# Optimization experiments

Measured on AMD Instinct MI355X. Metric: run time of the kernel, lower is better.

## Reference

```python
import jax, jax.numpy as jnp
import numpy as np

H = 8        # num_heads
DK = 128     # head_k_dim
DV = 128     # head_v_dim
HID = 1024   # hidden_size
CHUNK = 64   # chunk size for chunked linear attention
EPS = 1e-5


def setup_inputs() -> dict:
    key = jax.random.key(0)
    ks = jax.random.split(key, 16)
    s = 0.02
    inp = {
        "hidden_states": jax.random.normal(ks[0], (2, 8192, HID), dtype=jnp.float32),
        "Wq": jax.random.normal(ks[1], (HID, HID), dtype=jnp.float32) * s,
        "Wk": jax.random.normal(ks[2], (HID, HID), dtype=jnp.float32) * s,
        "Wv": jax.random.normal(ks[3], (HID, HID), dtype=jnp.float32) * s,
        "fmq_w1": jax.random.normal(ks[4], (DK, DK), dtype=jnp.float32) * s,
        "fmq_b1": jnp.zeros((DK,), dtype=jnp.float32),
        "fmq_w2": jax.random.normal(ks[5], (DK, DK), dtype=jnp.float32) * s,
        "fmq_b2": jnp.zeros((DK,), dtype=jnp.float32),
        "fmk_w1": jax.random.normal(ks[6], (DK, DK), dtype=jnp.float32) * s,
        "fmk_b1": jnp.zeros((DK,), dtype=jnp.float32),
        "fmk_w2": jax.random.normal(ks[7], (DK, DK), dtype=jnp.float32) * s,
        "fmk_b2": jnp.zeros((DK,), dtype=jnp.float32),
        "rms_w": jnp.ones((DV,), dtype=jnp.float32),
        "Wo": jax.random.normal(ks[8], (HID, HID), dtype=jnp.float32) * s,
    }
    return inp


def reference(hidden_states, Wq, Wk, Wv, fmq_w1, fmq_b1, fmq_w2, fmq_b2,
              fmk_w1, fmk_b1, fmk_w2, fmk_b2, rms_w, Wo):
    B, T, _ = hidden_states.shape
    scale = DK ** -0.5

    # projections (torch Linear: x @ W.T), split heads -> [B,T,H,D]
    q = (hidden_states @ Wq.T).reshape(B, T, H, DK)
    k = (hidden_states @ Wk.T).reshape(B, T, H, DK)
    v = (hidden_states @ Wv.T).reshape(B, T, H, DV)

    # Hadamard feature maps: l1(x) * l2(x)
    q = (q @ fmq_w1.T + fmq_b1) * (q @ fmq_w2.T + fmq_b2)
    k = (k @ fmk_w1.T + fmk_b1) * (k @ fmk_w2.T + fmk_b2)

    q = q * scale

    # chunked causal linear attention: o_t = q_t @ sum_{s<=t} k_s v_s^T
    N = T // CHUNK
    qc = q.reshape(B, N, CHUNK, H, DK)
    kc = k.reshape(B, N, CHUNK, H, DK)
    vc = v.reshape(B, N, CHUNK, H, DV)

    # per-chunk KV outer-product sums, exclusive prefix over chunks
    kv = jnp.einsum('bnchk,bnchv->bnhkv', kc, vc)
    S = jnp.cumsum(kv, axis=1) - kv  # state entering each chunk

    o_inter = jnp.einsum('bnchk,bnhkv->bnchv', qc, S)

    # intra-chunk causal part
    A = jnp.einsum('bnihk,bnjhk->bnhij', qc, kc)
    causal = jnp.tril(jnp.ones((CHUNK, CHUNK), dtype=bool))
    A = jnp.where(causal, A, 0.0)
    o_intra = jnp.einsum('bnhij,bnjhv->bnihv', A, vc)

    o = (o_inter + o_intra).reshape(B, T, H, DV)

    # RMSNorm over head_v_dim with affine weight
    o = o * jax.lax.rsqrt(jnp.mean(o * o, axis=-1, keepdims=True) + EPS) * rms_w

    o = o.reshape(B, T, H * DV) @ Wo.T
    return o
```

## Files before the change

kernel.cpp:

```cpp
#include <hip/hip_runtime.h>


typedef __bf16 bf16x8 __attribute__((ext_vector_type(8)));
typedef float  f32x4  __attribute__((ext_vector_type(4)));

__device__ __forceinline__ float bf2f(unsigned short u) {
  union { unsigned int i; float f; } v; v.i = ((unsigned int)u) << 16; return v.f;
}
__device__ __forceinline__ unsigned short f2bf(float f) {
  union { float f; unsigned int i; } v; v.f = f;
  return (unsigned short)((v.i + 0x8000u) >> 16);
}
__device__ __forceinline__ unsigned int pk2(float a, float b) {
  union { float f; unsigned int i; } x, y; x.f = a; y.f = b;
  return ((x.i + 0x8000u) >> 16) | ((y.i + 0x8000u) & 0xFFFF0000u);
}
__device__ __forceinline__ f32x4 mfma16(bf16x8 a, bf16x8 b, f32x4 c) {
  return __builtin_amdgcn_mfma_f32_16x16x32_bf16(a, b, c, 0, 0, 0);
}
__device__ __forceinline__ void gl_lds16(const unsigned short* g, unsigned short* l) {
  __builtin_amdgcn_global_load_lds((const __attribute__((address_space(1))) void*)g,
                                   (__attribute__((address_space(3))) void*)l, 16, 0, 0);
}

__global__ void __launch_bounds__(256)
cvt_kernel(const float* __restrict__ s, unsigned short* __restrict__ d, int n4) {
  const int i = blockIdx.x * 256 + threadIdx.x;
  if (i >= n4) return;
  const float4 f = ((const float4*)s)[i];
  uint2 o; o.x = pk2(f.x, f.y); o.y = pk2(f.z, f.w);
  ((uint2*)d)[i] = o;
}
__global__ void __launch_bounds__(256)
cvt4_kernel(const float* __restrict__ s0, const float* __restrict__ s1,
            const float* __restrict__ s2, const float* __restrict__ s3,
            unsigned short* __restrict__ d0, unsigned short* __restrict__ d1,
            unsigned short* __restrict__ d2, unsigned short* __restrict__ d3,
            int n4) {
  const int w = blockIdx.y;
  const float* s = (w == 0) ? s0 : (w == 1) ? s1 : (w == 2) ? s2 : s3;
  unsigned short* d = (w == 0) ? d0 : (w == 1) ? d1 : (w == 2) ? d2 : d3;
  const int i = blockIdx.x * 256 + threadIdx.x;
  if (i >= n4) return;
  const float4 f = ((const float4*)s)[i];
  uint2 o; o.x = pk2(f.x, f.y); o.y = pk2(f.z, f.w);
  ((uint2*)d)[i] = o;
}

__global__ void __launch_bounds__(256)
qkv_gemm(const unsigned short* __restrict__ Xb,
         const unsigned short* __restrict__ Wqb, const unsigned short* __restrict__ Wkb,
         const unsigned short* __restrict__ Wvb,
         unsigned short* __restrict__ Q, unsigned short* __restrict__ Kf,
         unsigned short* __restrict__ VT) {
  constexpr int K = 1024;
  __shared__ unsigned short As[128 * 32];
  __shared__ unsigned short Bs[128 * 32];
  const int tid = threadIdx.x;
  const int bx = blockIdx.x;
  const int rowBase = blockIdx.y * 128;
  const int sel = bx >> 3;
  const int colBase = (bx & 7) * 128;
  const unsigned short* Bw = (sel == 0) ? Wqb : ((sel == 1) ? Wkb : Wvb);

  const int lane = tid & 63, wid = tid >> 6;
  const int lq = lane & 15, quad = lane >> 4;
  const int wm = (wid >> 1) * 64, wn = (wid & 1) * 64;

  const int srow = wid * 32 + (lane >> 2);
  const int scol = (lane & 3) * 8;
  const unsigned short* gA = Xb + (size_t)(rowBase + srow) * K + scol;
  const unsigned short* gB = Bw + (size_t)(colBase + srow) * K + scol;
  unsigned short* lA0 = As + wid * 1024;
  unsigned short* lA1 = As + wid * 1024 + 512;
  unsigned short* lB0 = Bs + wid * 1024;
  unsigned short* lB1 = Bs + wid * 1024 + 512;

  f32x4 acc[4][4] = {};
  for (int kt = 0; kt < K / 32; ++kt) {
    __syncthreads();
    gl_lds16(gA + kt * 32, lA0);
    gl_lds16(gA + kt * 32 + 16 * K, lA1);
    gl_lds16(gB + kt * 32, lB0);
    gl_lds16(gB + kt * 32 + 16 * K, lB1);
    __syncthreads();
    bf16x8 af[4], bfr[4];
#pragma unroll
    for (int i = 0; i < 4; ++i)
      af[i] = *(const bf16x8*)(As + (wm + i * 16 + lq) * 32 + quad * 8);
#pragma unroll
    for (int j = 0; j < 4; ++j)
      bfr[j] = *(const bf16x8*)(Bs + (wn + j * 16 + lq) * 32 + quad * 8);
#pragma unroll
    for (int i = 0; i < 4; ++i)
#pragma unroll
      for (int j = 0; j < 4; ++j) acc[i][j] = mfma16(af[i], bfr[j], acc[i][j]);
  }
  if (sel < 2) {
    unsigned short* C = (sel == 0) ? Q : Kf;
#pragma unroll
    for (int i = 0; i < 4; ++i)
#pragma unroll
      for (int j = 0; j < 4; ++j) {
        const int col = colBase + wn + j * 16 + lq;
#pragma unroll
        for (int r = 0; r < 4; ++r) {
          const int row = rowBase + wm + i * 16 + quad * 4 + r;
          C[(size_t)row * 1024 + col] = f2bf(acc[i][j][r]);
        }
      }
  } else {
#pragma unroll
    for (int i = 0; i < 4; ++i)
#pragma unroll
      for (int j = 0; j < 4; ++j) {
        const int col = colBase + wn + j * 16 + lq;
        const int h = col >> 7, dv = col & 127;
        const int row0 = rowBase + wm + i * 16 + quad * 4;
        const int b = row0 >> 13, tl = row0 & 8191;
        ushort4 t4;
        t4.x = f2bf(acc[i][j][0]); t4.y = f2bf(acc[i][j][1]);
        t4.z = f2bf(acc[i][j][2]); t4.w = f2bf(acc[i][j][3]);
        *(ushort4*)(VT + (((size_t)(b * 8 + h) * 128 + dv) << 13) + tl) = t4;
      }
  }
}

__global__ void __launch_bounds__(256)
out_gemm(const unsigned short* __restrict__ A, const unsigned short* __restrict__ Bw,
         float* __restrict__ C) {
  constexpr int K = 1024;
  __shared__ unsigned short As[128 * 32];
  __shared__ unsigned short Bs[128 * 32];
  const int tid = threadIdx.x;
  const int rowBase = blockIdx.y * 128;
  const int colBase = blockIdx.x * 128;
  const int lane = tid & 63, wid = tid >> 6;
  const int lq = lane & 15, quad = lane >> 4;
  const int wm = (wid >> 1) * 64, wn = (wid & 1) * 64;

  const int srow = wid * 32 + (lane >> 2);
  const int scol = (lane & 3) * 8;
  const unsigned short* gA = A + (size_t)(rowBase + srow) * K + scol;
  const unsigned short* gB = Bw + (size_t)(colBase + srow) * K + scol;
  unsigned short* lA0 = As + wid * 1024;
  unsigned short* lA1 = As + wid * 1024 + 512;
  unsigned short* lB0 = Bs + wid * 1024;
  unsigned short* lB1 = Bs + wid * 1024 + 512;

  f32x4 acc[4][4] = {};
  for (int kt = 0; kt < K / 32; ++kt) {
    __syncthreads();
    gl_lds16(gA + kt * 32, lA0);
    gl_lds16(gA + kt * 32 + 16 * K, lA1);
    gl_lds16(gB + kt * 32, lB0);
    gl_lds16(gB + kt * 32 + 16 * K, lB1);
    __syncthreads();
    bf16x8 af[4], bfr[4];
#pragma unroll
    for (int i = 0; i < 4; ++i)
      af[i] = *(const bf16x8*)(As + (wm + i * 16 + lq) * 32 + quad * 8);
#pragma unroll
    for (int j = 0; j < 4; ++j)
      bfr[j] = *(const bf16x8*)(Bs + (wn + j * 16 + lq) * 32 + quad * 8);
#pragma unroll
    for (int i = 0; i < 4; ++i)
#pragma unroll
      for (int j = 0; j < 4; ++j) acc[i][j] = mfma16(af[i], bfr[j], acc[i][j]);
  }
#pragma unroll
  for (int i = 0; i < 4; ++i)
#pragma unroll
    for (int j = 0; j < 4; ++j) {
      const int col = colBase + wn + j * 16 + lq;
#pragma unroll
      for (int r = 0; r < 4; ++r) {
        const int row = rowBase + wm + i * 16 + quad * 4 + r;
        C[(size_t)row * 1024 + col] = acc[i][j][r];
      }
    }
}

__global__ void __launch_bounds__(256)
fm_kernel(unsigned short* __restrict__ Qb, unsigned short* __restrict__ Kb,
          const unsigned short* __restrict__ fq1b, const unsigned short* __restrict__ fq2b,
          const unsigned short* __restrict__ fk1b, const unsigned short* __restrict__ fk2b,
          const float* __restrict__ fqb1, const float* __restrict__ fqb2,
          const float* __restrict__ fkb1, const float* __restrict__ fkb2) {
  __shared__ unsigned short Aq[64 * 136];
  const int z = blockIdx.z;
  unsigned short* buf = z ? Kb : Qb;
  const unsigned short* w1b = z ? fk1b : fq1b;
  const unsigned short* w2b = z ? fk2b : fq2b;
  const float* b1 = z ? fkb1 : fqb1;
  const float* b2 = z ? fkb2 : fqb2;
  const float scale = z ? 1.0f : 0.08838834764831843f;

  const int tid = threadIdx.x;
  const int t0 = blockIdx.x * 256;
  const int h = blockIdx.y, hc = h * 128;
  const int lane = tid & 63, wid = tid >> 6, lq = lane & 15, quad = lane >> 4;
  const int wn = wid * 32;

  bf16x8 w1f[4][2], w2f[4][2];
#pragma unroll
  for (int ks = 0; ks < 4; ++ks)
#pragma unroll
    for (int j = 0; j < 2; ++j) {
      const int nr = wn + j * 16 + lq;
      w1f[ks][j] = *(const bf16x8*)(w1b + nr * 128 + ks * 32 + quad * 8);
      w2f[ks][j] = *(const bf16x8*)(w2b + nr * 128 + ks * 32 + quad * 8);
    }

  const float bb1[2] = { b1[wn + lq], b1[wn + 16 + lq] };
  const float bb2[2] = { b2[wn + lq], b2[wn + 16 + lq] };

  for (int tt = 0; tt < 4; ++tt) {
    const int tb = t0 + tt * 64;
#pragma unroll
    for (int it = 0; it < 4; ++it) {
      const int p = tid + it * 256;
      const int row = p >> 4, c8 = (p & 15) * 8;
      *(uint4*)(Aq + row * 136 + c8) =
          *(const uint4*)(buf + (size_t)(tb + row) * 1024 + hc + c8);
    }
    __syncthreads();
    f32x4 a1[4][2] = {}, a2[4][2] = {};
#pragma unroll
    for (int ks = 0; ks < 4; ++ks) {
      bf16x8 af[4];
#pragma unroll
      for (int i = 0; i < 4; ++i)
        af[i] = *(const bf16x8*)(Aq + (i * 16 + lq) * 136 + ks * 32 + quad * 8);
#pragma unroll
      for (int j = 0; j < 2; ++j)
#pragma unroll
        for (int i = 0; i < 4; ++i) {
          a1[i][j] = mfma16(af[i], w1f[ks][j], a1[i][j]);
          a2[i][j] = mfma16(af[i], w2f[ks][j], a2[i][j]);
        }
    }
    __syncthreads();
#pragma unroll
    for (int j = 0; j < 2; ++j) {
      const int col = wn + j * 16 + lq;
#pragma unroll
      for (int i = 0; i < 4; ++i)
#pragma unroll
        for (int r = 0; r < 4; ++r) {
          const float v = (a1[i][j][r] + bb1[j]) * (a2[i][j][r] + bb2[j]) * scale;
          buf[(size_t)(tb + i * 16 + quad * 4 + r) * 1024 + hc + col] = f2bf(v);
        }
    }
  }
}

__global__ void __launch_bounds__(256)
kv_kernel(const unsigned short* __restrict__ Kf, const unsigned short* __restrict__ VT,
          unsigned short* __restrict__ KV) {
  __shared__ unsigned short Kt[128 * 72];
  __shared__ unsigned short Vt[128 * 72];
  const int tid = threadIdx.x;
  const int n = blockIdx.x, bh = blockIdx.y;
  const int b = bh >> 3, h = bh & 7;
  const int t0g = b * 8192 + n * 64;
  const int tl0 = n * 64;
#pragma unroll
  for (int it = 0; it < 4; ++it) {
    const int p = tid + it * 256;
    const int d = p >> 3, c8 = (p & 7) * 8;
    *(uint4*)(Vt + d * 72 + c8) =
        *(const uint4*)(VT + (((size_t)bh * 128 + d) << 13) + tl0 + c8);
    const int tok = p >> 4, c8k = (p & 15) * 8;
    const unsigned short* src = Kf + (size_t)(t0g + tok) * 1024 + h * 128 + c8k;
    ushort4 k0 = *(const ushort4*)(src);
    ushort4 k1 = *(const ushort4*)(src + 4);
    Kt[(c8k + 0) * 72 + tok] = k0.x; Kt[(c8k + 1) * 72 + tok] = k0.y;
    Kt[(c8k + 2) * 72 + tok] = k0.z; Kt[(c8k + 3) * 72 + tok] = k0.w;
    Kt[(c8k + 4) * 72 + tok] = k1.x; Kt[(c8k + 5) * 72 + tok] = k1.y;
    Kt[(c8k + 6) * 72 + tok] = k1.z; Kt[(c8k + 7) * 72 + tok] = k1.w;
  }
  __syncthreads();
  const int lane = tid & 63, wid = tid >> 6, lq = lane & 15, quad = lane >> 4;
  const int wm = (wid >> 1) * 64, wn = (wid & 1) * 64;
  f32x4 acc[4][4] = {};
#pragma unroll
  for (int ks = 0; ks < 2; ++ks) {
    bf16x8 af[4], bfr[4];
#pragma unroll
    for (int i = 0; i < 4; ++i)
      af[i] = *(const bf16x8*)(Vt + (wm + i * 16 + lq) * 72 + ks * 32 + quad * 8);
#pragma unroll
    for (int j = 0; j < 4; ++j)
      bfr[j] = *(const bf16x8*)(Kt + (wn + j * 16 + lq) * 72 + ks * 32 + quad * 8);
#pragma unroll
    for (int i = 0; i < 4; ++i)
#pragma unroll
      for (int j = 0; j < 4; ++j) acc[i][j] = mfma16(af[i], bfr[j], acc[i][j]);
  }
  const size_t base = ((size_t)bh * 128 + n) * 16384;
#pragma unroll
  for (int i = 0; i < 4; ++i)
#pragma unroll
    for (int j = 0; j < 4; ++j)
#pragma unroll
      for (int r = 0; r < 4; ++r)
        KV[base + (size_t)(wm + i * 16 + quad * 4 + r) * 128 + wn + j * 16 + lq] =
            f2bf(acc[i][j][r]);
}

__global__ void __launch_bounds__(256)
cumsum_kernel(unsigned short* __restrict__ KV) {
  const int idx = blockIdx.x * 256 + threadIdx.x;
  const int bh = idx >> 14, e = idx & 16383;
  unsigned short* p = KV + (size_t)bh * (128 * 16384) + e;
  float run = 0.f;
  for (int n = 0; n < 128; ++n) {
    const float x = bf2f(*p);
    *p = f2bf(run);
    run += x;
    p += 16384;
  }
}

__global__ void __launch_bounds__(256)
attn_kernel(const unsigned short* __restrict__ Q, const unsigned short* __restrict__ Kf,
            const unsigned short* __restrict__ VT, const unsigned short* __restrict__ S,
            const float* __restrict__ rmsw, unsigned short* __restrict__ O) {
  __shared__ uint4 smem4[3968];
  unsigned short* sm = (unsigned short*)smem4;
  unsigned short* SQ = sm;
  unsigned short* KS = sm + 8704;
  unsigned short* VTl = sm + 17920;
  unsigned short* AL = sm + 27136;
  float* OL = (float*)sm;
  float* RED = (float*)AL;
  float* SCL = RED + 256;

  const int tid = threadIdx.x;
  const int n = blockIdx.x, bh = blockIdx.y;
  const int b = bh >> 3, h = bh & 7;
  const int t0g = b * 8192 + n * 64;
  const int tl0 = n * 64;
  const int lane = tid & 63, wid = tid >> 6, lq = lane & 15, quad = lane >> 4;

#pragma unroll
  for (int it = 0; it < 4; ++it) {
    const int p = tid + it * 256;
    const int row = p >> 4, c8 = (p & 15) * 8;
    *(uint4*)(SQ + row * 136 + c8) =
        *(const uint4*)(Q + (size_t)(t0g + row) * 1024 + h * 128 + c8);
    *(uint4*)(KS + row * 136 + c8) =
        *(const uint4*)(Kf + (size_t)(t0g + row) * 1024 + h * 128 + c8);
    const int d = p >> 3, c8b = (p & 7) * 8;
    *(uint4*)(VTl + d * 72 + c8b) =
        *(const uint4*)(VT + (((size_t)bh * 128 + d) << 13) + tl0 + c8b);
  }
  __syncthreads();

  {
    f32x4 aa[4] = {};
#pragma unroll
    for (int ks = 0; ks < 4; ++ks) {
      bf16x8 kf = *(const bf16x8*)(KS + (wid * 16 + lq) * 136 + ks * 32 + quad * 8);
#pragma unroll
      for (int i = 0; i < 4; ++i) {
        bf16x8 qf = *(const bf16x8*)(SQ + (i * 16 + lq) * 136 + ks * 32 + quad * 8);
        aa[i] = mfma16(qf, kf, aa[i]);
      }
    }
#pragma unroll
    for (int i = 0; i < 4; ++i)
#pragma unroll
      for (int r = 0; r < 4; ++r) {
        const int qp = i * 16 + quad * 4 + r, kp = wid * 16 + lq;
        AL[qp * 72 + kp] = f2bf(kp <= qp ? aa[i][r] : 0.f);
      }
  }
  __syncthreads();

  const size_t sbase = ((size_t)bh * 128 + n) * 16384;
#pragma unroll
  for (int it = 0; it < 4; ++it) {
    const int p = tid + it * 256;
    const int dv = p >> 3, c8 = (p & 7) * 8;
    *(uint4*)(KS + dv * 72 + c8) = *(const uint4*)(S + sbase + (size_t)dv * 128 + c8);
  }
  __syncthreads();

  f32x4 oa[4][2] = {};
#pragma unroll
  for (int ks = 0; ks < 2; ++ks) {
    bf16x8 bv[2], sf[2];
#pragma unroll
    for (int j = 0; j < 2; ++j) {
      bv[j] = *(const bf16x8*)(VTl + (wid * 32 + j * 16 + lq) * 72 + ks * 32 + quad * 8);
      sf[j] = *(const bf16x8*)(KS + (wid * 32 + j * 16 + lq) * 72 + ks * 32 + quad * 8);
    }
#pragma unroll
    for (int i = 0; i < 4; ++i) {
      bf16x8 af = *(const bf16x8*)(AL + (i * 16 + lq) * 72 + ks * 32 + quad * 8);
      bf16x8 qf = *(const bf16x8*)(SQ + (i * 16 + lq) * 136 + ks * 32 + quad * 8);
#pragma unroll
      for (int j = 0; j < 2; ++j) {
        oa[i][j] = mfma16(af, bv[j], oa[i][j]);
        oa[i][j] = mfma16(qf, sf[j], oa[i][j]);
      }
    }
  }
  __syncthreads();

#pragma unroll
  for (int it = 0; it < 4; ++it) {
    const int p = tid + it * 256;
    const int dv = p >> 3, c8 = (p & 7) * 8;
    *(uint4*)(KS + dv * 72 + c8) =
        *(const uint4*)(S + sbase + (size_t)dv * 128 + 64 + c8);
  }
  __syncthreads();

#pragma unroll
  for (int ks = 0; ks < 2; ++ks) {
    bf16x8 sf[2];
#pragma unroll
    for (int j = 0; j < 2; ++j)
      sf[j] = *(const bf16x8*)(KS + (wid * 32 + j * 16 + lq) * 72 + ks * 32 + quad * 8);
#pragma unroll
    for (int i = 0; i < 4; ++i) {
      bf16x8 qf = *(const bf16x8*)(SQ + (i * 16 + lq) * 136 + (ks + 2) * 32 + quad * 8);
#pragma unroll
      for (int j = 0; j < 2; ++j) oa[i][j] = mfma16(qf, sf[j], oa[i][j]);
    }
  }
  __syncthreads();

#pragma unroll
  for (int i = 0; i < 4; ++i)
#pragma unroll
    for (int j = 0; j < 2; ++j)
#pragma unroll
      for (int r = 0; r < 4; ++r)
        OL[(i * 16 + quad * 4 + r) * 132 + wid * 32 + j * 16 + lq] = oa[i][j][r];
  __syncthreads();

  {
    const int r = tid >> 2, part = tid & 3;
    const float* pr = OL + r * 132 + part * 32;
    float s = 0.f;
#pragma unroll
    for (int c = 0; c < 32; ++c) { const float v = pr[c]; s += v * v; }
    RED[r * 4 + part] = s;
  }
  __syncthreads();
  if (tid < 64) {
    const float ms = (RED[tid * 4] + RED[tid * 4 + 1] + RED[tid * 4 + 2] + RED[tid * 4 + 3]) *
                     (1.f / 128.f);
    SCL[tid] = rsqrtf(ms + 1e-5f);
  }
  __syncthreads();

#pragma unroll
  for (int it = 0; it < 4; ++it) {
    const int r = (tid >> 4) + it * 16;
    const int c8 = (tid & 15) * 8;
    const float sc = SCL[r];
    unsigned short us[8];
#pragma unroll
    for (int e = 0; e < 8; ++e)
      us[e] = f2bf(OL[r * 132 + c8 + e] * sc * rmsw[c8 + e]);
    uint4 pk;
    pk.x = (unsigned int)us[0] | ((unsigned int)us[1] << 16);
    pk.y = (unsigned int)us[2] | ((unsigned int)us[3] << 16);
    pk.z = (unsigned int)us[4] | ((unsigned int)us[5] << 16);
    pk.w = (unsigned int)us[6] | ((unsigned int)us[7] << 16);
    *(uint4*)(O + (size_t)(t0g + r) * 1024 + h * 128 + c8) = pk;
  }
}

extern "C" void kernel_launch(void* const* d_in, const int* in_sizes, int n_in,
                              void* d_out, int out_size, void* d_ws, size_t ws_size,
                              hipStream_t stream) {
  const float* X    = (const float*)d_in[0];
  const float* Wq   = (const float*)d_in[1];
  const float* Wk   = (const float*)d_in[2];
  const float* Wv   = (const float*)d_in[3];
  const float* fq1  = (const float*)d_in[4];
  const float* fqb1 = (const float*)d_in[5];
  const float* fq2  = (const float*)d_in[6];
  const float* fqb2 = (const float*)d_in[7];
  const float* fk1  = (const float*)d_in[8];
  const float* fkb1 = (const float*)d_in[9];
  const float* fk2  = (const float*)d_in[10];
  const float* fkb2 = (const float*)d_in[11];
  const float* rmsw = (const float*)d_in[12];
  const float* Wo   = (const float*)d_in[13];

  const size_t MB = 1u << 20;
  char* ws = (char*)d_ws;
  unsigned short* Q    = (unsigned short*)(ws);
  unsigned short* Kf   = (unsigned short*)(ws + 32 * MB);
  unsigned short* VT   = (unsigned short*)(ws + 64 * MB);
  unsigned short* KV   = (unsigned short*)(ws + 96 * MB);
  unsigned short* Xb   = KV;
  unsigned short* Wqb  = (unsigned short*)(ws + 160 * MB);
  unsigned short* Wkb  = (unsigned short*)(ws + 162 * MB);
  unsigned short* Wvb  = (unsigned short*)(ws + 164 * MB);
  unsigned short* Wob  = (unsigned short*)(ws + 166 * MB);
  unsigned short* fq1b = (unsigned short*)(ws + 168 * MB);
  unsigned short* fq2b = fq1b + 16384;
  unsigned short* fk1b = fq1b + 32768;
  unsigned short* fk2b = fq1b + 49152;
  unsigned short* O    = Q;

  cvt4_kernel<<<dim3(1024, 4), 256, 0, stream>>>(Wq, Wk, Wv, Wo,
                                                 Wqb, Wkb, Wvb, Wob, 262144);
  cvt4_kernel<<<dim3(16, 4), 256, 0, stream>>>(fq1, fq2, fk1, fk2,
                                               fq1b, fq2b, fk1b, fk2b, 4096);
  cvt_kernel<<<16384, 256, 0, stream>>>(X, Xb, 4194304);

  qkv_gemm<<<dim3(24, 128), 256, 0, stream>>>(Xb, Wqb, Wkb, Wvb, Q, Kf, VT);
  fm_kernel<<<dim3(64, 8, 2), 256, 0, stream>>>(Q, Kf, fq1b, fq2b, fk1b, fk2b,
                                                fqb1, fqb2, fkb1, fkb2);
  kv_kernel<<<dim3(128, 16), 256, 0, stream>>>(Kf, VT, KV);
  cumsum_kernel<<<1024, 256, 0, stream>>>(KV);
  attn_kernel<<<dim3(128, 16), 256, 0, stream>>>(Q, Kf, VT, KV, rmsw, O);
  out_gemm<<<dim3(8, 128), 256, 0, stream>>>(O, Wob, (float*)d_out);
}
```

Baseline: 450.6 us.

## Replace QKV and output GEMMs with 256x256 tiles and multi-stage async LDS pipeline

```diff
diff --git a/kernel.cpp b/kernel.cpp
--- a/kernel.cpp
+++ b/kernel.cpp
@@ -1,5 +1,4 @@
 #include <hip/hip_runtime.h>
-
 
 typedef __bf16 bf16x8 __attribute__((ext_vector_type(8)));
 typedef float  f32x4  __attribute__((ext_vector_type(4)));
@@ -47,136 +46,164 @@
   ((uint2*)d)[i] = o;
 }
 
-__global__ void __launch_bounds__(256)
-qkv_gemm(const unsigned short* __restrict__ Xb,
-         const unsigned short* __restrict__ Wqb, const unsigned short* __restrict__ Wkb,
-         const unsigned short* __restrict__ Wvb,
-         unsigned short* __restrict__ Q, unsigned short* __restrict__ Kf,
-         unsigned short* __restrict__ VT) {
-  constexpr int K = 1024;
-  __shared__ unsigned short As[128 * 32];
-  __shared__ unsigned short Bs[128 * 32];
-  const int tid = threadIdx.x;
-  const int bx = blockIdx.x;
-  const int rowBase = blockIdx.y * 128;
-  const int sel = bx >> 3;
-  const int colBase = (bx & 7) * 128;
-  const unsigned short* Bw = (sel == 0) ? Wqb : ((sel == 1) ? Wkb : Wvb);
-
+__device__ __forceinline__ int stage_goff(int s) {
+  const int j = s >> 3, c = (s & 7) ^ (j & 7);
+  return (2 * j + (c >> 2)) * 1024 + (c & 3) * 8;
+}
+
+__device__ __forceinline__ void gemm256_loop(const unsigned short* __restrict__ gA,
+                                             const unsigned short* __restrict__ gB,
+                                             unsigned short* __restrict__ ldsA,
+                                             unsigned short* __restrict__ ldsB,
+                                             int tid, f32x4 (&acc)[8][4]) {
   const int lane = tid & 63, wid = tid >> 6;
   const int lq = lane & 15, quad = lane >> 4;
-  const int wm = (wid >> 1) * 64, wn = (wid & 1) * 64;
-
-  const int srow = wid * 32 + (lane >> 2);
-  const int scol = (lane & 3) * 8;
-  const unsigned short* gA = Xb + (size_t)(rowBase + srow) * K + scol;
-  const unsigned short* gB = Bw + (size_t)(colBase + srow) * K + scol;
-  unsigned short* lA0 = As + wid * 1024;
-  unsigned short* lA1 = As + wid * 1024 + 512;
-  unsigned short* lB0 = Bs + wid * 1024;
-  unsigned short* lB1 = Bs + wid * 1024 + 512;
-
-  f32x4 acc[4][4] = {};
-  for (int kt = 0; kt < K / 32; ++kt) {
-    __syncthreads();
-    gl_lds16(gA + kt * 32, lA0);
-    gl_lds16(gA + kt * 32 + 16 * K, lA1);
-    gl_lds16(gB + kt * 32, lB0);
-    gl_lds16(gB + kt * 32 + 16 * K, lB1);
-    __syncthreads();
+  const int wm = (wid >> 2) * 128, wn = (wid & 3) * 64;
+
+  const unsigned short* gA0 = gA + stage_goff(tid);
+  const unsigned short* gA1 = gA + stage_goff(512 + tid);
+  const unsigned short* gB0 = gB + stage_goff(tid);
+  const unsigned short* gB1 = gB + stage_goff(512 + tid);
+  const int l0 = wid * 512;
+  const int l1 = 4096 + wid * 512;
+  const int soff = (lq >> 1) * 64 + (((((lq & 1) << 2) + quad) ^ ((lq >> 1) & 7))) * 8;
+
+#pragma unroll
+  for (int h = 0; h < 3; ++h) {
+    gl_lds16(gA0 + h * 32, ldsA + h * 8192 + l0);
+    gl_lds16(gA1 + h * 32, ldsA + h * 8192 + l1);
+    gl_lds16(gB0 + h * 32, ldsB + h * 8192 + l0);
+    gl_lds16(gB1 + h * 32, ldsB + h * 8192 + l1);
+  }
+  asm volatile("s_waitcnt vmcnt(8)" ::: "memory");
+  __builtin_amdgcn_s_barrier();
+  __builtin_amdgcn_sched_barrier(0);
+
+#pragma unroll
+  for (int u = 0; u < 32; ++u) {
+    const unsigned short* A8 = ldsA + (u & 3) * 8192;
+    const unsigned short* B8 = ldsB + (u & 3) * 8192;
+    unsigned short* sa = ldsA + ((u + 3) & 3) * 8192;
+    unsigned short* sb = ldsB + ((u + 3) & 3) * 8192;
     bf16x8 af[4], bfr[4];
-#pragma unroll
-    for (int i = 0; i < 4; ++i)
-      af[i] = *(const bf16x8*)(As + (wm + i * 16 + lq) * 32 + quad * 8);
-#pragma unroll
-    for (int j = 0; j < 4; ++j)
-      bfr[j] = *(const bf16x8*)(Bs + (wn + j * 16 + lq) * 32 + quad * 8);
-#pragma unroll
-    for (int i = 0; i < 4; ++i)
-#pragma unroll
-      for (int j = 0; j < 4; ++j) acc[i][j] = mfma16(af[i], bfr[j], acc[i][j]);
-  }
+    if (u < 29) {
+      gl_lds16(gA0 + (u + 3) * 32, sa + l0);
+      gl_lds16(gA1 + (u + 3) * 32, sa + l1);
+    }
+#pragma unroll
+    for (int f = 0; f < 4; ++f)
+      af[f] = *(const bf16x8*)(A8 + (wm + f * 16) * 32 + soff);
+#pragma unroll
+    for (int g = 0; g < 4; ++g)
+      bfr[g] = *(const bf16x8*)(B8 + (wn + g * 16) * 32 + soff);
+    __builtin_amdgcn_s_barrier();
+    __builtin_amdgcn_s_setprio(1);
+#pragma unroll
+    for (int f = 0; f < 4; ++f)
+#pragma unroll
+      for (int g = 0; g < 4; ++g) acc[f][g] = mfma16(af[f], bfr[g], acc[f][g]);
+    __builtin_amdgcn_s_setprio(0);
+    if (u < 29) {
+      gl_lds16(gB0 + (u + 3) * 32, sb + l0);
+      gl_lds16(gB1 + (u + 3) * 32, sb + l1);
+    }
+#pragma unroll
+    for (int f = 0; f < 4; ++f)
+      af[f] = *(const bf16x8*)(A8 + (wm + 64 + f * 16) * 32 + soff);
+    __builtin_amdgcn_s_barrier();
+    __builtin_amdgcn_s_setprio(1);
+#pragma unroll
+    for (int f = 0; f < 4; ++f)
+#pragma unroll
+      for (int g = 0; g < 4; ++g) acc[f + 4][g] = mfma16(af[f], bfr[g], acc[f + 4][g]);
+    __builtin_amdgcn_s_setprio(0);
+    __builtin_amdgcn_sched_barrier(0);
+    if (u < 31) {
+      if (u < 29)       asm volatile("s_waitcnt vmcnt(8)" ::: "memory");
+      else if (u == 29) asm volatile("s_waitcnt vmcnt(4)" ::: "memory");
+      else              asm volatile("s_waitcnt vmcnt(0)" ::: "memory");
+      __builtin_amdgcn_s_barrier();
+      __builtin_amdgcn_sched_barrier(0);
+    }
+  }
+}
+
+__global__ void __launch_bounds__(512, 2)
+qkv_gemm256(const unsigned short* __restrict__ Xb,
+            const unsigned short* __restrict__ Wqb, const unsigned short* __restrict__ Wkb,
+            const unsigned short* __restrict__ Wvb,
+            unsigned short* __restrict__ Q, unsigned short* __restrict__ Kf,
+            unsigned short* __restrict__ VT) {
+  extern __shared__ unsigned short lds[];
+  const int tid = threadIdx.x;
+  const int l = (blockIdx.x & 7) * 96 + (blockIdx.x >> 3);
+  const int tm = l & 63, ct = l >> 6;
+  const int sel = ct >> 2;
+  const int rowBase = tm * 256, colBase = (ct & 3) * 256;
+  const unsigned short* Bw = (sel == 0) ? Wqb : ((sel == 1) ? Wkb : Wvb);
+
+  f32x4 acc[8][4] = {};
+  gemm256_loop(Xb + (size_t)rowBase * 1024, Bw + (size_t)colBase * 1024,
+               lds, lds + 32768, tid, acc);
+
+  const int lane = tid & 63, wid = tid >> 6;
+  const int lq = lane & 15, quad = lane >> 4;
+  const int wm = (wid >> 2) * 128, wn = (wid & 3) * 64;
   if (sel < 2) {
     unsigned short* C = (sel == 0) ? Q : Kf;
 #pragma unroll
-    for (int i = 0; i < 4; ++i)
-#pragma unroll
-      for (int j = 0; j < 4; ++j) {
-        const int col = colBase + wn + j * 16 + lq;
+    for (int f = 0; f < 8; ++f)
+#pragma unroll
+      for (int g = 0; g < 4; ++g) {
+        const int col = colBase + wn + g * 16 + lq;
 #pragma unroll
         for (int r = 0; r < 4; ++r) {
-          const int row = rowBase + wm + i * 16 + quad * 4 + r;
-          C[(size_t)row * 1024 + col] = f2bf(acc[i][j][r]);
+          const int row = rowBase + wm + f * 16 + quad * 4 + r;
+          C[(size_t)row * 1024 + col] = f2bf(acc[f][g][r]);
         }
       }
   } else {
 #pragma unroll
-    for (int i = 0; i < 4; ++i)
-#pragma unroll
-      for (int j = 0; j < 4; ++j) {
-        const int col = colBase + wn + j * 16 + lq;
+    for (int f = 0; f < 8; ++f)
+#pragma unroll
+      for (int g = 0; g < 4; ++g) {
+        const int col = colBase + wn + g * 16 + lq;
         const int h = col >> 7, dv = col & 127;
-        const int row0 = rowBase + wm + i * 16 + quad * 4;
+        const int row0 = rowBase + wm + f * 16 + quad * 4;
         const int b = row0 >> 13, tl = row0 & 8191;
         ushort4 t4;
-        t4.x = f2bf(acc[i][j][0]); t4.y = f2bf(acc[i][j][1]);
-        t4.z = f2bf(acc[i][j][2]); t4.w = f2bf(acc[i][j][3]);
+        t4.x = f2bf(acc[f][g][0]); t4.y = f2bf(acc[f][g][1]);
+        t4.z = f2bf(acc[f][g][2]); t4.w = f2bf(acc[f][g][3]);
         *(ushort4*)(VT + (((size_t)(b * 8 + h) * 128 + dv) << 13) + tl) = t4;
       }
   }
 }
 
-__global__ void __launch_bounds__(256)
-out_gemm(const unsigned short* __restrict__ A, const unsigned short* __restrict__ Bw,
-         float* __restrict__ C) {
-  constexpr int K = 1024;
-  __shared__ unsigned short As[128 * 32];
-  __shared__ unsigned short Bs[128 * 32];
+__global__ void __launch_bounds__(512, 2)
+out_gemm256(const unsigned short* __restrict__ A, const unsigned short* __restrict__ Bw,
+            float* __restrict__ C) {
+  extern __shared__ unsigned short lds[];
   const int tid = threadIdx.x;
-  const int rowBase = blockIdx.y * 128;
-  const int colBase = blockIdx.x * 128;
+  const int l = (blockIdx.x & 7) * 32 + (blockIdx.x >> 3);
+  const int tm = l & 63, tn = l >> 6;
+  const int rowBase = tm * 256, colBase = tn * 256;
+
+  f32x4 acc[8][4] = {};
+  gemm256_loop(A + (size_t)rowBase * 1024, Bw + (size_t)colBase * 1024,
+               lds, lds + 32768, tid, acc);
+
   const int lane = tid & 63, wid = tid >> 6;
   const int lq = lane & 15, quad = lane >> 4;
-  const int wm = (wid >> 1) * 64, wn = (wid & 1) * 64;
-
-  const int srow = wid * 32 + (lane >> 2);
-  const int scol = (lane & 3) * 8;
-  const unsigned short* gA = A + (size_t)(rowBase + srow) * K + scol;
-  const unsigned short* gB = Bw + (size_t)(colBase + srow) * K + scol;
-  unsigned short* lA0 = As + wid * 1024;
-  unsigned short* lA1 = As + wid * 1024 + 512;
-  unsigned short* lB0 = Bs + wid * 1024;
-  unsigned short* lB1 = Bs + wid * 1024 + 512;
-
-  f32x4 acc[4][4] = {};
-  for (int kt = 0; kt < K / 32; ++kt) {
-    __syncthreads();
-    gl_lds16(gA + kt * 32, lA0);
-    gl_lds16(gA + kt * 32 + 16 * K, lA1);
-    gl_lds16(gB + kt * 32, lB0);
-    gl_lds16(gB + kt * 32 + 16 * K, lB1);
-    __syncthreads();
-    bf16x8 af[4], bfr[4];
-#pragma unroll
-    for (int i = 0; i < 4; ++i)
-      af[i] = *(const bf16x8*)(As + (wm + i * 16 + lq) * 32 + quad * 8);
-#pragma unroll
-    for (int j = 0; j < 4; ++j)
-      bfr[j] = *(const bf16x8*)(Bs + (wn + j * 16 + lq) * 32 + quad * 8);
-#pragma unroll
-    for (int i = 0; i < 4; ++i)
-#pragma unroll
-      for (int j = 0; j < 4; ++j) acc[i][j] = mfma16(af[i], bfr[j], acc[i][j]);
-  }
-#pragma unroll
-  for (int i = 0; i < 4; ++i)
-#pragma unroll
-    for (int j = 0; j < 4; ++j) {
-      const int col = colBase + wn + j * 16 + lq;
+  const int wm = (wid >> 2) * 128, wn = (wid & 3) * 64;
+#pragma unroll
+  for (int f = 0; f < 8; ++f)
+#pragma unroll
+    for (int g = 0; g < 4; ++g) {
+      const int col = colBase + wn + g * 16 + lq;
 #pragma unroll
       for (int r = 0; r < 4; ++r) {
-        const int row = rowBase + wm + i * 16 + quad * 4 + r;
-        C[(size_t)row * 1024 + col] = acc[i][j][r];
+        const int row = rowBase + wm + f * 16 + quad * 4 + r;
+        C[(size_t)row * 1024 + col] = acc[f][g][r];
       }
     }
 }
@@ -495,6 +522,15 @@
   const float* rmsw = (const float*)d_in[12];
   const float* Wo   = (const float*)d_in[13];
 
+  static bool attr_done = false;
+  if (!attr_done) {
+    (void)hipFuncSetAttribute((const void*)qkv_gemm256,
+                              hipFuncAttributeMaxDynamicSharedMemorySize, 131072);
+    (void)hipFuncSetAttribute((const void*)out_gemm256,
+                              hipFuncAttributeMaxDynamicSharedMemorySize, 131072);
+    attr_done = true;
+  }
+
   const size_t MB = 1u << 20;
   char* ws = (char*)d_ws;
   unsigned short* Q    = (unsigned short*)(ws);
@@ -518,11 +554,11 @@
                                                fq1b, fq2b, fk1b, fk2b, 4096);
   cvt_kernel<<<16384, 256, 0, stream>>>(X, Xb, 4194304);
 
-  qkv_gemm<<<dim3(24, 128), 256, 0, stream>>>(Xb, Wqb, Wkb, Wvb, Q, Kf, VT);
+  qkv_gemm256<<<dim3(768), dim3(512), 131072, stream>>>(Xb, Wqb, Wkb, Wvb, Q, Kf, VT);
   fm_kernel<<<dim3(64, 8, 2), 256, 0, stream>>>(Q, Kf, fq1b, fq2b, fk1b, fk2b,
                                                 fqb1, fqb2, fkb1, fkb2);
   kv_kernel<<<dim3(128, 16), 256, 0, stream>>>(Kf, VT, KV);
   cumsum_kernel<<<1024, 256, 0, stream>>>(KV);
   attn_kernel<<<dim3(128, 16), 256, 0, stream>>>(Q, Kf, VT, KV, rmsw, O);
-  out_gemm<<<dim3(8, 128), 256, 0, stream>>>(O, Wob, (float*)d_out);
-}
+  out_gemm256<<<dim3(256), dim3(512), 131072, stream>>>(O, Wob, (float*)d_out);
+}
```

Result: faster. 439.0 us (-2.6%).
